# Performance work log

Measured on AMD Instinct MI355X. Metric: run time of the kernel, lower is better.

Reference implementation:

```python
import jax, jax.numpy as jnp
import numpy as np

H = 256    # hidden_size
CVQ = 64   # vq_ph_channel
K = 128    # vq_ph_codebook_dim
NL = 5     # num_layers per ConvBlocks
NB = 2     # layers_in_block
KS = 3     # kernel_size


def _ln_c(x, g, b, eps=1e-5):
    # LayerNorm over channel dim of a [B, C, T] tensor
    m = jnp.mean(x, axis=1, keepdims=True)
    v = jnp.mean((x - m) ** 2, axis=1, keepdims=True)
    return (x - m) * jax.lax.rsqrt(v + eps) * g[None, :, None] + b[None, :, None]


def _causal_conv(x, w, b):
    # x [B,Cin,T], w [Cout,Cin,K]; left (causal) padding of K-1
    y = jax.lax.conv_general_dilated(x, w, (1,), [(w.shape[-1] - 1, 0)],
                                     dimension_numbers=('NCH', 'OIH', 'NCH'))
    return y + b[None, :, None]


def _pw(x, w, b):
    # pointwise (kernel-size-1) conv: w [Cout, Cin]
    return jnp.einsum('oi,bit->bot', w, x) + b[None, :, None]


def _conv_blocks(x, mask, ln_g, ln_b, w1, b1, w2, b2, last_g, last_b, post_w, post_b):
    # LeftPadConvBlocks: NL residual blocks x NB sub-blocks of
    # LN -> causal conv (C->2C, k=3) -> *k^-0.5 -> GELU -> 1x1 conv (2C->C), residual + mask
    scale = KS ** -0.5
    for i in range(NL):
        for j in range(NB):
            h = _ln_c(x, ln_g[i, j], ln_b[i, j])
            h = _causal_conv(h, w1[i, j], b1[i, j]) * scale
            h = jax.nn.gelu(h, approximate=False)
            h = _pw(h, w2[i, j], b2[i, j])
            x = (x + h) * mask
    x = _ln_c(x, last_g, last_b) * mask
    x = _causal_conv(x, post_w, post_b) * mask
    return x


def _group_by_segs(h_bct, mel2ph, L):
    # scatter-mean mel frames into phoneme segments; index 0 = padding (dropped)
    h = jnp.swapaxes(h_bct, 1, 2)  # [B, T, H]
    def one(hb, mb):
        s = jnp.zeros((L + 1, hb.shape[-1]), hb.dtype).at[mb].add(hb)
        c = jnp.zeros((L + 1,), hb.dtype).at[mb].add(1.0)
        return s[1:] / jnp.clip(c[1:], 1.0)[:, None]
    g = jax.vmap(one)(h, mel2ph)   # [B, L, H]
    return jnp.swapaxes(g, 1, 2)   # [B, H, L]


def _vq(z, codebook, beta=0.25):
    # EMA-VQ forward math: nearest-codebook lookup + straight-through + commitment loss
    x = jnp.swapaxes(z, 1, 2)                                # [B, T, C]
    d = (jnp.sum(x ** 2, -1, keepdims=True)
         - 2.0 * jnp.einsum('btc,kc->btk', x, codebook)
         + jnp.sum(codebook ** 2, -1))                       # [B, T, K]
    idx = jnp.argmin(d, axis=-1)                             # [B, T]
    q = codebook[idx]                                        # [B, T, C]
    loss = beta * jnp.mean((x - jax.lax.stop_gradient(q)) ** 2)
    q_st = x + jax.lax.stop_gradient(q - x)
    return jnp.swapaxes(q_st, 1, 2), loss, idx


def setup_inputs() -> dict:
    key = jax.random.key(0)
    ks = list(jax.random.split(key, 64))
    it = iter(ks)
    B, T, L = 16, 2048, 512
    f = lambda shape, s: jax.random.normal(next(it), shape, jnp.float32) * s
    inp = {}
    inp['x'] = jax.random.normal(next(it), (B, 80, T), jnp.float32)
    inp['in_nonpadding'] = jnp.ones((B, 1, T), jnp.float32)
    inp['in_mel2ph'] = jnp.sort(jax.random.randint(next(it), (B, T), 1, L + 1), axis=-1)
    inp['ph_nonpadding'] = jnp.ones((B, 1, L), jnp.float32)
    inp['conv_in_w'] = f((H, 80), 0.05)
    inp['conv_in_b'] = jnp.zeros((H,), jnp.float32)
    for p in ('enc', 'pn'):
        inp[p + '_ln_g'] = jnp.ones((NL, NB, H), jnp.float32)
        inp[p + '_ln_b'] = jnp.zeros((NL, NB, H), jnp.float32)
        inp[p + '_w1'] = f((NL, NB, 2 * H, H, KS), 0.03)
        inp[p + '_b1'] = jnp.zeros((NL, NB, 2 * H), jnp.float32)
        inp[p + '_w2'] = f((NL, NB, H, 2 * H), 0.03)
        inp[p + '_b2'] = jnp.zeros((NL, NB, H), jnp.float32)
        inp[p + '_last_g'] = jnp.ones((H,), jnp.float32)
        inp[p + '_last_b'] = jnp.zeros((H,), jnp.float32)
        inp[p + '_post_w'] = f((H, H, KS), 0.03)
        inp[p + '_post_b'] = jnp.zeros((H,), jnp.float32)
    inp['proj_in_w'] = f((CVQ, H), 0.05)
    inp['proj_in_b'] = jnp.zeros((CVQ,), jnp.float32)
    inp['proj_out_w'] = f((H, CVQ), 0.05)
    inp['proj_out_b'] = jnp.zeros((H,), jnp.float32)
    inp['codebook'] = f((K, CVQ), 0.1)
    return inp


def reference(x, in_nonpadding, in_mel2ph, ph_nonpadding,
              conv_in_w, conv_in_b,
              enc_ln_g, enc_ln_b, enc_w1, enc_b1, enc_w2, enc_b2,
              enc_last_g, enc_last_b, enc_post_w, enc_post_b,
              pn_ln_g, pn_ln_b, pn_w1, pn_b1, pn_w2, pn_b2,
              pn_last_g, pn_last_b, pn_post_w, pn_post_b,
              proj_in_w, proj_in_b, proj_out_w, proj_out_b, codebook):
    L = ph_nonpadding.shape[-1]
    h = _pw(x, conv_in_w, conv_in_b) * in_nonpadding                     # ph_conv_in
    h = _conv_blocks(h, in_nonpadding, enc_ln_g, enc_ln_b, enc_w1, enc_b1,
                     enc_w2, enc_b2, enc_last_g, enc_last_b,
                     enc_post_w, enc_post_b) * in_nonpadding             # ph_encoder
    h = _group_by_segs(h, in_mel2ph, L)                                  # [B, H, L]
    h = _conv_blocks(h, ph_nonpadding, pn_ln_g, pn_ln_b, pn_w1, pn_b1,
                     pn_w2, pn_b2, pn_last_g, pn_last_b,
                     pn_post_w, pn_post_b) * ph_nonpadding               # ph_postnet
    z = _pw(h, proj_in_w, proj_in_b)                                     # ph_latents_proj_in
    q, vq_loss, idx = _vq(z, codebook)                                   # VQ
    out = _pw(q, proj_out_w, proj_out_b)                                 # ph_latents_proj_out
    return out, vq_loss, idx
```

## Files before the change

kernel.cpp:

```cpp
#include <hip/hip_runtime.h>
#include <hip/hip_bf16.h>


typedef unsigned short u16;
typedef unsigned int u32;
typedef __attribute__((ext_vector_type(8))) _Float16 f16x8;
typedef __attribute__((ext_vector_type(16))) float f32x16;

#define OUT_LOSS_OFF 2097152
#define OUT_IDX_OFF  2097153

__device__ __forceinline__ void split_f16(float x, u16& h, u16& l) {
    union { _Float16 f; u16 u; } a, b;
    a.f = (_Float16)x;
    float hf = (float)a.f;
    b.f = (_Float16)(x - hf);
    h = a.u; l = b.u;
}

__global__ __launch_bounds__(256) void k_t_mat(const float* __restrict__ w,
                                               float* __restrict__ wt,
                                               int G, int O, int I) {
    size_t n = (size_t)G * O * I;
    for (size_t i = (size_t)blockIdx.x * 256 + threadIdx.x; i < n;
         i += (size_t)gridDim.x * 256) {
        int ci = (int)(i % I);
        int o  = (int)((i / I) % O);
        int g  = (int)(i / ((size_t)I * O));
        wt[((size_t)g * I + ci) * O + o] = w[i];
    }
}

__global__ __launch_bounds__(256) void k_t_w1mf(const float* __restrict__ w,
                                                u16* __restrict__ BH,
                                                u16* __restrict__ BL, int S) {
    size_t N = (size_t)S * 3 * 16 * 16 * 64 * 8;
    for (size_t i = (size_t)blockIdx.x * 256 + threadIdx.x; i < N;
         i += (size_t)gridDim.x * 256) {
        int j = (int)(i & 7); size_t r = i >> 3;
        int L = (int)(r & 63); r >>= 6;
        int nt = (int)(r & 15); r >>= 4;
        int kb = (int)(r & 15); r >>= 4;
        int k3 = (int)(r % 3); int s = (int)(r / 3);
        int oc = nt * 32 + (L & 31);
        int c = kb * 16 + ((L >> 5) << 3) + j;
        float v = w[(((size_t)s * 512 + oc) * 256 + c) * 3 + k3];
        u16 h, l; split_f16(v, h, l);
        BH[i] = h; BL[i] = l;
    }
}

__global__ __launch_bounds__(256) void k_t_w2mf(const float* __restrict__ w,
                                                u16* __restrict__ BH,
                                                u16* __restrict__ BL, int S) {
    size_t N = (size_t)S * 32 * 8 * 64 * 8;
    for (size_t i = (size_t)blockIdx.x * 256 + threadIdx.x; i < N;
         i += (size_t)gridDim.x * 256) {
        int j = (int)(i & 7);
        int L = (int)((i >> 3) & 63);
        int nt = (int)((i >> 9) & 7);
        int kb = (int)((i >> 12) & 31);
        int s = (int)(i >> 17);
        int oc = nt * 32 + (L & 31);
        int ic = kb * 16 + ((L >> 5) << 3) + j;
        float v = w[((size_t)s * 256 + oc) * 512 + ic];
        u16 h, l; split_f16(v, h, l);
        BH[i] = h; BL[i] = l;
    }
}

// ... 18 lines not shown
                                            const float* __restrict__ wt,
                                            const float* __restrict__ bias,
                                            const float* __restrict__ mask,
                                            float* __restrict__ y,
                                            float* __restrict__ MM,
                                            float* __restrict__ IV, int T) {
    extern __shared__ float X[];
    constexpr int NG = COUT / CHUNK;
    __shared__ float rs[64 * NG], rs2[64 * NG];
    const int b = blockIdx.y, t0 = blockIdx.x * 64;
    for (int i = threadIdx.x; i < CIN * 64; i += 256) {
        int ci = i >> 6, j = i & 63;
        X[i] = x[((size_t)b * CIN + ci) * T + t0 + j];
    }
    __syncthreads();
    const int tl = threadIdx.x & 63;
    const int g = __builtin_amdgcn_readfirstlane((int)(threadIdx.x >> 6));
    float acc[CHUNK];
#pragma unroll
    for (int o = 0; o < CHUNK; o++) acc[o] = 0.f;
    for (int i = 0; i < CIN; i++) {
        float xv = X[i * 64 + tl];
        const float* wr = wt + (size_t)i * COUT + g * CHUNK;
#pragma unroll
        for (int o = 0; o < CHUNK; o++) acc[o] = fmaf(wr[o], xv, acc[o]);
    }
    float mk = mask ? mask[(size_t)b * T + t0 + tl] : 1.0f;
    float s = 0.f, s2 = 0.f;
#pragma unroll
    for (int o = 0; o < CHUNK; o++) {
        int oc = g * CHUNK + o;
        float val = (acc[o] + bias[oc]) * mk;
        y[((size_t)b * COUT + oc) * T + t0 + tl] = val;
        s += val; s2 += val * val;
    }
    if constexpr (STATS) {
        rs[g * 64 + tl] = s; rs2[g * 64 + tl] = s2;
        __syncthreads();
        if (threadIdx.x < 64) {
            float ss = 0.f, ss2 = 0.f;
#pragma unroll
            for (int gg = 0; gg < NG; gg++) {
                ss += rs[gg * 64 + threadIdx.x];
                ss2 += rs2[gg * 64 + threadIdx.x];
            }
            float m = ss * (1.0f / COUT);
            float var = ss2 * (1.0f / COUT) - m * m;
            MM[(size_t)b * T + t0 + threadIdx.x] = m;
            IV[(size_t)b * T + t0 + threadIdx.x] = 1.0f / sqrtf(var + 1e-5f);
        }
    }
}

template <int M>
__global__ __launch_bounds__(512, 4) void k_sub(
    const float* __restrict__ xin, float* __restrict__ xout,
    const float* __restrict__ MMi, const float* __restrict__ IVi,
    const float* __restrict__ lng, const float* __restrict__ lnb,
    const u16* __restrict__ B1H, const u16* __restrict__ B1L,
    const float* __restrict__ b1,
    const u16* __restrict__ B2H, const u16* __restrict__ B2L,
    const float* __restrict__ b2, const float* __restrict__ mask,
    float* __restrict__ MMo, float* __restrict__ IVo, int T) {
    constexpr int MT = M / 32;
    constexpr int SH = (M + 2) * 264 * 2;
    constexpr int CG = 512 / M;
    constexpr int CPT = 256 / CG;
    __shared__ __align__(16) char smem[2 * SH + 4096];
    u16* LH = (u16*)smem;
    u16* LL = (u16*)(smem + SH);
    u16* GH = (u16*)smem;
    u16* GL = (u16*)(smem + SH);
    float* SOUT = (float*)smem;
    float* rs  = (float*)(smem + 2 * SH);
    float* rs2 = (float*)(smem + 2 * SH + 2048);

    const int tid = threadIdx.x;
    const int b = blockIdx.y, t0 = blockIdx.x * M;
    const size_t xoff = (size_t)b * 256 * T;
    const size_t bT = (size_t)b * T;

    {
        int jj = tid & (M - 1);
        int cg = tid / M;
        int t = t0 - 2 + jj;
        bool ok = (t >= 0);
        float m = ok ? MMi[bT + t] : 0.f;
        float v = ok ? IVi[bT + t] : 0.f;
#pragma unroll
        for (int i = 0; i < CPT; i++) {
            int c = cg + i * CG;
            float xv = ok ? xin[xoff + (size_t)c * T + t] : 0.f;
            float ln = ok ? ((xv - m) * v * lng[c] + lnb[c]) : 0.f;
            u16 h, l; split_f16(ln, h, l);
            LH[jj * 264 + c] = h; LL[jj * 264 + c] = l;
        }
        int j2 = M + (tid >> 8);
        int c2 = tid & 255;
        int t2 = t0 + (M - 2) + (tid >> 8);
        float m2 = MMi[bT + t2], v2 = IVi[bT + t2];
        float x2 = xin[xoff + (size_t)c2 * T + t2];
        float ln2 = (x2 - m2) * v2 * lng[c2] + lnb[c2];
        u16 h2, l2; split_f16(ln2, h2, l2);
        LH[j2 * 264 + c2] = h2; LL[j2 * 264 + c2] = l2;
    }
    __syncthreads();

    const int lane = tid & 63;
    const int w = tid >> 6;
    const int arow = lane & 31;
    const int acol = (lane >> 5) << 3;
    const int thalf = (lane >> 5) << 2;
    const float ks = 0.5773502691896258f;
    const int oc_l = w * 32 + (lane & 31);
    const u16* b1h0 = B1H + (size_t)w * 512 + (size_t)lane * 8;
    const u16* b1l0 = B1L + (size_t)w * 512 + (size_t)lane * 8;
    const u16* b1h1 = B1H + (size_t)(8 + w) * 512 + (size_t)lane * 8;
    const u16* b1l1 = B1L + (size_t)(8 + w) * 512 + (size_t)lane * 8;
    const u16* b2h = B2H + (size_t)w * 512 + (size_t)lane * 8;
    const u16* b2l = B2L + (size_t)w * 512 + (size_t)lane * 8;

    f32x16 c0[MT], c1[MT];
#pragma unroll
    for (int m = 0; m < MT; m++)
#pragma unroll
        for (int r = 0; r < 16; r++) { c0[m][r] = 0.f; c1[m][r] = 0.f; }
    __builtin_amdgcn_s_setprio(1);
#pragma unroll 2
    for (int kk = 0; kk < 48; kk++) {
        int k3 = kk >> 4, kb = kk & 15;
        f16x8 bh0 = *(const f16x8*)(b1h0 + (size_t)kk * 8192);
        f16x8 bl0 = *(const f16x8*)(b1l0 + (size_t)kk * 8192);
        f16x8 bh1 = *(const f16x8*)(b1h1 + (size_t)kk * 8192);
        f16x8 bl1 = *(const f16x8*)(b1l1 + (size_t)kk * 8192);
#pragma unroll
        for (int m = 0; m < MT; m++) {
            int ao = (m * 32 + arow + k3) * 264 + kb * 16 + acol;
            f16x8 ah = *(const f16x8*)&LH[ao];
            f16x8 al = *(const f16x8*)&LL[ao];
            c0[m] = __builtin_amdgcn_mfma_f32_32x32x16_f16(ah, bh0, c0[m], 0, 0, 0);
            c1[m] = __builtin_amdgcn_mfma_f32_32x32x16_f16(ah, bh1, c1[m], 0, 0, 0);
            c0[m] = __builtin_amdgcn_mfma_f32_32x32x16_f16(ah, bl0, c0[m], 0, 0, 0);
            c1[m] = __builtin_amdgcn_mfma_f32_32x32x16_f16(ah, bl1, c1[m], 0, 0, 0);
            c0[m] = __builtin_amdgcn_mfma_f32_32x32x16_f16(al, bh0, c0[m], 0, 0, 0);
            c1[m] = __builtin_amdgcn_mfma_f32_32x32x16_f16(al, bh1, c1[m], 0, 0, 0);
        }
    }
    __builtin_amdgcn_s_setprio(0);
    __syncthreads();

    {
        float bb = b1[oc_l];
#pragma unroll
        for (int m = 0; m < MT; m++)
#pragma unroll
            for (int r = 0; r < 16; r++) {
                int trow = m * 32 + thalf + ((r >> 2) << 3) + (r & 3);
                float y = (c0[m][r] + bb) * ks;
                float ge = 0.5f * y * (1.0f + erff(y * 0.7071067811865476f));
                u16 h, l; split_f16(ge, h, l);
                GH[trow * 264 + oc_l] = h; GL[trow * 264 + oc_l] = l;
            }
    }
    __syncthreads();

#pragma unroll
    for (int m = 0; m < MT; m++)
#pragma unroll
        for (int r = 0; r < 16; r++) c0[m][r] = 0.f;
    __builtin_amdgcn_s_setprio(1);
#pragma unroll 2
    for (int i = 0; i < 16; i++) {
        f16x8 bh2 = *(const f16x8*)(b2h + (size_t)i * 4096);
        f16x8 bl2 = *(const f16x8*)(b2l + (size_t)i * 4096);
#pragma unroll
        for (int m = 0; m < MT; m++) {
            int go = (m * 32 + arow) * 264 + i * 16 + acol;
            f16x8 gh = *(const f16x8*)&GH[go];
            f16x8 gl = *(const f16x8*)&GL[go];
            c0[m] = __builtin_amdgcn_mfma_f32_32x32x16_f16(gh, bh2, c0[m], 0, 0, 0);
            c0[m] = __builtin_amdgcn_mfma_f32_32x32x16_f16(gh, bl2, c0[m], 0, 0, 0);
            c0[m] = __builtin_amdgcn_mfma_f32_32x32x16_f16(gl, bh2, c0[m], 0, 0, 0);
        }
    }
    __builtin_amdgcn_s_setprio(0);
    __syncthreads();

    {
        float bb = b1[256 + oc_l];
#pragma unroll
        for (int m = 0; m < MT; m++)
#pragma unroll
            for (int r = 0; r < 16; r++) {
                int trow = m * 32 + thalf + ((r >> 2) << 3) + (r & 3);
                float y = (c1[m][r] + bb) * ks;
                float ge = 0.5f * y * (1.0f + erff(y * 0.7071067811865476f));
                u16 h, l; split_f16(ge, h, l);
                GH[trow * 264 + oc_l] = h; GL[trow * 264 + oc_l] = l;
            }
    }
    __syncthreads();

    __builtin_amdgcn_s_setprio(1);
#pragma unroll 2
    for (int i = 0; i < 16; i++) {
        f16x8 bh2 = *(const f16x8*)(b2h + (size_t)(16 + i) * 4096);
        f16x8 bl2 = *(const f16x8*)(b2l + (size_t)(16 + i) * 4096);
#pragma unroll
        for (int m = 0; m < MT; m++) {
            int go = (m * 32 + arow) * 264 + i * 16 + acol;
            f16x8 gh = *(const f16x8*)&GH[go];
            f16x8 gl = *(const f16x8*)&GL[go];
            c0[m] = __builtin_amdgcn_mfma_f32_32x32x16_f16(gh, bh2, c0[m], 0, 0, 0);
            c0[m] = __builtin_amdgcn_mfma_f32_32x32x16_f16(gh, bl2, c0[m], 0, 0, 0);
            c0[m] = __builtin_amdgcn_mfma_f32_32x32x16_f16(gl, bh2, c0[m], 0, 0, 0);
        }
    }
    __builtin_amdgcn_s_setprio(0);
    __syncthreads();

#pragma unroll
    for (int m = 0; m < MT; m++)
#pragma unroll
        for (int r = 0; r < 16; r++) {
            int trow = m * 32 + thalf + ((r >> 2) << 3) + (r & 3);
            SOUT[trow * 260 + oc_l] = c0[m][r];
        }
    __syncthreads();
    {
        int t = tid & (M - 1), cg = tid / M;
        float mk = mask[bT + t0 + t];
        float s = 0.f, s2 = 0.f;
#pragma unroll
        for (int i = 0; i < CPT; i++) {
            int c = cg * CPT + i;
            size_t adr = xoff + (size_t)c * T + t0 + t;
            float val = (xin[adr] + SOUT[t * 260 + c] + b2[c]) * mk;
            xout[adr] = val;
            s += val; s2 += val * val;
        }
        rs[tid] = s; rs2[tid] = s2;
    }
    __syncthreads();
    if (tid < M) {
        float ss = 0.f, ss2 = 0.f;
#pragma unroll
        for (int k = 0; k < CG; k++) {
            ss += rs[k * M + tid]; ss2 += rs2[k * M + tid];
        }
        float m = ss * (1.0f / 256.0f);
        float var = ss2 * (1.0f / 256.0f) - m * m;
        MMo[bT + t0 + tid] = m;
        IVo[bT + t0 + tid] = 1.0f / sqrtf(var + 1e-5f);
    }
}

__global__ __launch_bounds__(1024, 4) void k_sub16(
    const float* __restrict__ xin, float* __restrict__ xout,
    const float* __restrict__ MMi, const float* __restrict__ IVi,
    const float* __restrict__ lng, const float* __restrict__ lnb,
    const u16* __restrict__ B1H, const u16* __restrict__ B1L,
    const float* __restrict__ b1,
    const u16* __restrict__ B2H, const u16* __restrict__ B2L,
    const float* __restrict__ b2, const float* __restrict__ mask,
    float* __restrict__ MMo, float* __restrict__ IVo, int T) {
    __shared__ __align__(16) char smem[44096];
    u16* LH = (u16*)smem;
    u16* LL = (u16*)(smem + 17952);
    u16* GH = (u16*)smem;
    u16* GL = (u16*)(smem + 17952);
    float* SOUT = (float*)smem;
    float* rs  = (float*)(smem + 35904);
    float* rs2 = (float*)(smem + 40000);

    const int tid = threadIdx.x;
    const int b = blockIdx.y, t0 = blockIdx.x * 32;
    const size_t xoff = (size_t)b * 256 * T;
    const size_t bT = (size_t)b * T;

    {
        int jj = tid & 31;
        int cg = tid >> 5;
        int t = t0 - 2 + jj;
        bool ok = (t >= 0);
        float m = ok ? MMi[bT + t] : 0.f;
        float v = ok ? IVi[bT + t] : 0.f;
#pragma unroll
        for (int i = 0; i < 8; i++) {
            int c = cg + i * 32;
            float xv = ok ? xin[xoff + (size_t)c * T + t] : 0.f;
            float ln = ok ? ((xv - m) * v * lng[c] + lnb[c]) : 0.f;
            u16 h, l; split_f16(ln, h, l);
            LH[jj * 264 + c] = h; LL[jj * 264 + c] = l;
        }
        if (tid < 512) {
            int j2 = 32 + (tid >> 8);
            int c2 = tid & 255;
            int t2 = t0 + 30 + (tid >> 8);
            float ln2 = (xin[xoff + (size_t)c2 * T + t2] - MMi[bT + t2]) *
                        IVi[bT + t2] * lng[c2] + lnb[c2];
            u16 h2, l2; split_f16(ln2, h2, l2);
            LH[j2 * 264 + c2] = h2; LL[j2 * 264 + c2] = l2;
        }
    }
    __syncthreads();

    const int lane = tid & 63;
    const int w = tid >> 6;
    const int arow = lane & 31;
    const int acol = (lane >> 5) << 3;
    const int thalf = (lane >> 5) << 2;
    const float ks = 0.5773502691896258f;
    const int oc_l = w * 32 + (lane & 31);
    const u16* b1h = B1H + (size_t)w * 512 + (size_t)lane * 8;
    const u16* b1l = B1L + (size_t)w * 512 + (size_t)lane * 8;

    f32x16 cc;
#pragma unroll
    for (int r = 0; r < 16; r++) cc[r] = 0.f;
    __builtin_amdgcn_s_setprio(1);
#pragma unroll 4
    for (int kk = 0; kk < 48; kk++) {
        int k3 = kk >> 4, kb = kk & 15;
        int ao = (arow + k3) * 264 + kb * 16 + acol;
        f16x8 ah = *(const f16x8*)&LH[ao];
        f16x8 al = *(const f16x8*)&LL[ao];
        f16x8 bh = *(const f16x8*)(b1h + (size_t)kk * 8192);
        f16x8 bl = *(const f16x8*)(b1l + (size_t)kk * 8192);
        cc = __builtin_amdgcn_mfma_f32_32x32x16_f16(ah, bh, cc, 0, 0, 0);
        cc = __builtin_amdgcn_mfma_f32_32x32x16_f16(ah, bl, cc, 0, 0, 0);
        cc = __builtin_amdgcn_mfma_f32_32x32x16_f16(al, bh, cc, 0, 0, 0);
    }
    __builtin_amdgcn_s_setprio(0);
    __syncthreads();

    u32 preg[16];
    {
        float bb = b1[oc_l];
        if (w < 8) {
#pragma unroll
            for (int r = 0; r < 16; r++) {
                int trow = thalf + ((r >> 2) << 3) + (r & 3);
                float y = (cc[r] + bb) * ks;
                float ge = 0.5f * y * (1.0f + erff(y * 0.7071067811865476f));
                u16 h, l; split_f16(ge, h, l);
                GH[trow * 264 + oc_l] = h; GL[trow * 264 + oc_l] = l;
            }
        } else {
#pragma unroll
            for (int r = 0; r < 16; r++) {
                float y = (cc[r] + bb) * ks;
                float ge = 0.5f * y * (1.0f + erff(y * 0.7071067811865476f));
                u16 h, l; split_f16(ge, h, l);
                preg[r] = ((u32)h << 16) | (u32)l;
            }
        }
    }
    __syncthreads();

    const u16* b2h = B2H + (size_t)(w & 7) * 512 + (size_t)lane * 8;
    const u16* b2l = B2L + (size_t)(w & 7) * 512 + (size_t)lane * 8;
    if (w < 8) {
#pragma unroll
        for (int r = 0; r < 16; r++) cc[r] = 0.f;
        __builtin_amdgcn_s_setprio(1);
#pragma unroll 2
        for (int i = 0; i < 16; i++) {
            int go = arow * 264 + i * 16 + acol;
            f16x8 gh = *(const f16x8*)&GH[go];
            f16x8 gl = *(const f16x8*)&GL[go];
            f16x8 bh2 = *(const f16x8*)(b2h + (size_t)i * 4096);
            f16x8 bl2 = *(const f16x8*)(b2l + (size_t)i * 4096);
            cc = __builtin_amdgcn_mfma_f32_32x32x16_f16(gh, bh2, cc, 0, 0, 0);
            cc = __builtin_amdgcn_mfma_f32_32x32x16_f16(gh, bl2, cc, 0, 0, 0);
            cc = __builtin_amdgcn_mfma_f32_32x32x16_f16(gl, bh2, cc, 0, 0, 0);
        }
        __builtin_amdgcn_s_setprio(0);
    }
    __syncthreads();

    if (w >= 8) {
        int col = oc_l - 256;
#pragma unroll
        for (int r = 0; r < 16; r++) {
            int trow = thalf + ((r >> 2) << 3) + (r & 3);
            GH[trow * 264 + col] = (u16)(preg[r] >> 16);
            GL[trow * 264 + col] = (u16)(preg[r] & 0xffff);
        }
    }
    __syncthreads();

    if (w < 8) {
        __builtin_amdgcn_s_setprio(1);
#pragma unroll 2
        for (int i = 0; i < 16; i++) {
            int go = arow * 264 + i * 16 + acol;
            f16x8 gh = *(const f16x8*)&GH[go];
            f16x8 gl = *(const f16x8*)&GL[go];
            f16x8 bh2 = *(const f16x8*)(b2h + (size_t)(16 + i) * 4096);
            f16x8 bl2 = *(const f16x8*)(b2l + (size_t)(16 + i) * 4096);
            cc = __builtin_amdgcn_mfma_f32_32x32x16_f16(gh, bh2, cc, 0, 0, 0);
            cc = __builtin_amdgcn_mfma_f32_32x32x16_f16(gh, bl2, cc, 0, 0, 0);
            cc = __builtin_amdgcn_mfma_f32_32x32x16_f16(gl, bh2, cc, 0, 0, 0);
        }
        __builtin_amdgcn_s_setprio(0);
    }
    __syncthreads();

    if (w < 8) {
#pragma unroll
        for (int r = 0; r < 16; r++) {
            int trow = thalf + ((r >> 2) << 3) + (r & 3);
            SOUT[trow * 260 + oc_l] = cc[r];
        }
    }
    __syncthreads();
    {
        int t = tid & 31, cg = tid >> 5;
        float mk = mask[bT + t0 + t];
        float s = 0.f, s2 = 0.f;
#pragma unroll
        for (int i = 0; i < 8; i++) {
            int c = cg * 8 + i;
            size_t adr = xoff + (size_t)c * T + t0 + t;
            float val = (xin[adr] + SOUT[t * 260 + c] + b2[c]) * mk;
            xout[adr] = val;
            s += val; s2 += val * val;
        }
        rs[tid] = s; rs2[tid] = s2;
    }
    __syncthreads();
    if (tid < 32) {
        float ss = 0.f, ss2 = 0.f;
#pragma unroll
        for (int k = 0; k < 32; k++) {
            ss += rs[k * 32 + tid]; ss2 += rs2[k * 32 + tid];
        }
        float m = ss * (1.0f / 256.0f);
        float var = ss2 * (1.0f / 256.0f) - m * m;
        MMo[bT + t0 + tid] = m;
        IVo[bT + t0 + tid] = 1.0f / sqrtf(var + 1e-5f);
    }
}

template <int M>
__global__ __launch_bounds__(512, (M == 32 ? 8 : 4)) void k_lnc(
    const float* __restrict__ xin, float* __restrict__ xout,
    const float* __restrict__ MM, const float* __restrict__ IV,
    const float* __restrict__ lg, const float* __restrict__ lb,
    const u16* __restrict__ BH, const u16* __restrict__ BL,
    const float* __restrict__ bias, const float* __restrict__ mask, int T) {
    constexpr int MT = M / 32;
    constexpr int SH = (M + 2) * 264 * 2;
    constexpr int CG = 512 / M;
    constexpr int CPT = 256 / CG;
    __shared__ __align__(16) char smem[2 * SH];
    u16* LH = (u16*)smem;
    u16* LL = (u16*)(smem + SH);
    float* SOUT = (float*)smem;

    const int tid = threadIdx.x;
    const int b = blockIdx.y, t0 = blockIdx.x * M;
    const size_t xoff = (size_t)b * 256 * T;
    const size_t bT = (size_t)b * T;

    {
// ... 242 lines not shown
    const float* proj_out_b = (const float*)d_in[29];
    const float* codebook   = (const float*)d_in[30];
    float* out = (float*)d_out;

    float* ws = (float*)d_ws;
    float* A      = ws;
    float* Bb     = A + 8388608;
    float* CINT   = Bb + 8388608;
    float* PINT   = CINT + 20480;
    float* POUTT  = PINT + 16384;
    float* Z      = POUTT + 16384;
    float* MM0    = Z + 524288;
    float* IV0    = MM0 + 32768;
    float* MM1    = IV0 + 32768;
    float* IV1    = MM1 + 32768;
    int*   CNT    = (int*)(IV1 + 32768);
    int*   IDX    = CNT + 8192;
    float* LOSS   = (float*)(IDX + 8192);
    u16*   BH1E   = (u16*)(LOSS + 64);
    u16*   BL1E   = BH1E + 3932160;
    u16*   BH1P   = BL1E + 3932160;
    u16*   BL1P   = BH1P + 3932160;
    u16*   BH2E   = BL1P + 3932160;
    u16*   BL2E   = BH2E + 1310720;
    u16*   BH2P   = BL2E + 1310720;
    u16*   BL2P   = BH2P + 1310720;
    u16*   PH_E   = BL2P + 1310720;
    u16*   PL_E   = PH_E + 196608;
    u16*   PH_P   = PL_E + 196608;
    u16*   PL_P   = PH_P + 196608;

    k_t_w1mf<<<dim3(4096), dim3(256), 0, stream>>>(e_w1, BH1E, BL1E, 10);
    k_t_w1mf<<<dim3(4096), dim3(256), 0, stream>>>(p_w1, BH1P, BL1P, 10);
    k_t_w2mf<<<dim3(2048), dim3(256), 0, stream>>>(e_w2, BH2E, BL2E, 10);
    k_t_w2mf<<<dim3(2048), dim3(256), 0, stream>>>(p_w2, BH2P, BL2P, 10);
    k_t_wpmf<<<dim3(768),  dim3(256), 0, stream>>>(e_pw, PH_E, PL_E);
    k_t_wpmf<<<dim3(768),  dim3(256), 0, stream>>>(p_pw, PH_P, PL_P);
    k_t_mat  <<<dim3(80),  dim3(256), 0, stream>>>(conv_in_w, CINT, 1, 256, 80);
    k_t_mat  <<<dim3(64),  dim3(256), 0, stream>>>(proj_in_w, PINT, 1, 64, 256);
    k_t_mat  <<<dim3(64),  dim3(256), 0, stream>>>(proj_out_w, POUTT, 1, 256, 64);

    const size_t sm_scat = 256 * 65 * sizeof(float) + 64 * sizeof(int);

    k_pw<80, 256, 64, true><<<dim3(32, 16), dim3(256), 80 * 64 * 4, stream>>>(
        x, CINT, conv_in_b, in_np, A, MM0, IV0, 2048);

    float* cur = A;
    float* nxt = Bb;
    for (int s = 0; s < 10; s++) {
        float* mi = (s & 1) ? MM1 : MM0;
        float* vi = (s & 1) ? IV1 : IV0;
        float* mo = (s & 1) ? MM0 : MM1;
        float* vo = (s & 1) ? IV0 : IV1;
        k_sub<64><<<dim3(32, 16), dim3(512), 0, stream>>>(
            cur, nxt, mi, vi, e_ln_g + s * 256, e_ln_b + s * 256,
            BH1E + (size_t)s * 393216, BL1E + (size_t)s * 393216, e_b1 + s * 512,
            BH2E + (size_t)s * 131072, BL2E + (size_t)s * 131072, e_b2 + s * 256,
            in_np, mo, vo, 2048);
        float* t = cur; cur = nxt; nxt = t;
    }
    k_lnc<64><<<dim3(32, 16), dim3(512), 0, stream>>>(
        cur, nxt, MM0, IV0, e_lg, e_lb, PH_E, PL_E, e_pb, in_np, 2048);

    hipMemsetAsync(A, 0, (size_t)2097152 * 4, stream);
    hipMemsetAsync(LOSS, 0, 4, stream);
    k_counts<<<dim3(16), dim3(256), 0, stream>>>(mel2ph, CNT);
    k_scatter<<<dim3(32, 16), dim3(256), sm_scat, stream>>>(Bb, mel2ph, A);
    k_postprep<<<dim3(16), dim3(512), 0, stream>>>(A, CNT, MM0, IV0);

    cur = A; nxt = Bb;
    for (int s = 0; s < 10; s++) {
        float* mi = (s & 1) ? MM1 : MM0;
        float* vi = (s & 1) ? IV1 : IV0;
        float* mo = (s & 1) ? MM0 : MM1;
        float* vo = (s & 1) ? IV0 : IV1;
        k_sub16<<<dim3(16, 16), dim3(1024), 0, stream>>>(
            cur, nxt, mi, vi, p_ln_g + s * 256, p_ln_b + s * 256,
            BH1P + (size_t)s * 393216, BL1P + (size_t)s * 393216, p_b1 + s * 512,
            BH2P + (size_t)s * 131072, BL2P + (size_t)s * 131072, p_b2 + s * 256,
            ph_np, mo, vo, 512);
        float* t = cur; cur = nxt; nxt = t;
    }
    k_lnc<32><<<dim3(16, 16), dim3(512), 0, stream>>>(
        cur, nxt, MM0, IV0, p_lg, p_lb, PH_P, PL_P, p_pb, ph_np, 512);

    k_pw<256, 64, 16, false><<<dim3(8, 16), dim3(256), 256 * 64 * 4, stream>>>(
        Bb, PINT, proj_in_b, nullptr, Z, nullptr, nullptr, 512);

    k_vq<<<dim3(32), dim3(256), 0, stream>>>(Z, codebook, IDX, out, LOSS);
    k_loss<<<dim3(1), dim3(64), 0, stream>>>(LOSS, out);
    k_projout<<<dim3(8, 16), dim3(256), 0, stream>>>(codebook, IDX, POUTT,
                                                     proj_out_b, out);
}
```

Measured before the change: 2.119 ms.

## Interleave GELU packing with MFMA phases and split second GEMM across all waves

The 64-row sub-block kernel is specialised and reordered so the GELU and f16 hi/lo packing of one accumulator tile runs inside the MFMA loop that computes the next tile. This overlaps transcendental and LDS-store work with matrix-core work and removes separate barrier-delimited GELU passes. The 32-row kernel now stores the whole 512-wide GELU output in LDS and has all 16 waves do half of the K reduction of the 1x1 conv, adding the partials in LDS, instead of leaving half the waves idle. In exchange, the 32-row kernel's LDS footprint grows, which can lower blocks per CU, and it adds an extra accumulate pass through LDS.

```diff
diff --git a/kernel.cpp b/kernel.cpp
--- a/kernel.cpp
+++ b/kernel.cpp
@@ -16,6 +16,15 @@
     float hf = (float)a.f;
     b.f = (_Float16)(x - hf);
     h = a.u; l = b.u;
+}
+
+__device__ __forceinline__ void gelu_pack(float v, float bb, u16* GH, u16* GL,
+                                          int off) {
+    const float ks = 0.5773502691896258f;
+    float y = (v + bb) * ks;
+    float ge = 0.5f * y * (1.0f + erff(y * 0.7071067811865476f));
+    u16 h, l; split_f16(ge, h, l);
+    GH[off] = h; GL[off] = l;
 }
 
 __global__ __launch_bounds__(256) void k_t_mat(const float* __restrict__ w,
@@ -140,8 +149,7 @@
     }
 }
 
-template <int M>
-__global__ __launch_bounds__(512, 4) void k_sub(
+__global__ __launch_bounds__(512, 4) void k_sub64(
     const float* __restrict__ xin, float* __restrict__ xout,
     const float* __restrict__ MMi, const float* __restrict__ IVi,
     const float* __restrict__ lng, const float* __restrict__ lnb,
@@ -150,42 +158,38 @@
     const u16* __restrict__ B2H, const u16* __restrict__ B2L,
     const float* __restrict__ b2, const float* __restrict__ mask,
     float* __restrict__ MMo, float* __restrict__ IVo, int T) {
-    constexpr int MT = M / 32;
-    constexpr int SH = (M + 2) * 264 * 2;
-    constexpr int CG = 512 / M;
-    constexpr int CPT = 256 / CG;
-    __shared__ __align__(16) char smem[2 * SH + 4096];
+    __shared__ __align__(16) char smem[73792];
     u16* LH = (u16*)smem;
-    u16* LL = (u16*)(smem + SH);
+    u16* LL = (u16*)(smem + 34848);
     u16* GH = (u16*)smem;
-    u16* GL = (u16*)(smem + SH);
+    u16* GL = (u16*)(smem + 34848);
     float* SOUT = (float*)smem;
-    float* rs  = (float*)(smem + 2 * SH);
-    float* rs2 = (float*)(smem + 2 * SH + 2048);
+    float* rs  = (float*)(smem + 69696);
+    float* rs2 = (float*)(smem + 71744);
 
     const int tid = threadIdx.x;
-    const int b = blockIdx.y, t0 = blockIdx.x * M;
+    const int b = blockIdx.y, t0 = blockIdx.x * 64;
     const size_t xoff = (size_t)b * 256 * T;
     const size_t bT = (size_t)b * T;
 
     {
-        int jj = tid & (M - 1);
-        int cg = tid / M;
+        int jj = tid & 63;
+        int cg = tid >> 6;
         int t = t0 - 2 + jj;
         bool ok = (t >= 0);
         float m = ok ? MMi[bT + t] : 0.f;
         float v = ok ? IVi[bT + t] : 0.f;
 #pragma unroll
-        for (int i = 0; i < CPT; i++) {
-            int c = cg + i * CG;
+        for (int i = 0; i < 32; i++) {
+            int c = cg + i * 8;
             float xv = ok ? xin[xoff + (size_t)c * T + t] : 0.f;
             float ln = ok ? ((xv - m) * v * lng[c] + lnb[c]) : 0.f;
             u16 h, l; split_f16(ln, h, l);
             LH[jj * 264 + c] = h; LL[jj * 264 + c] = l;
         }
-        int j2 = M + (tid >> 8);
+        int j2 = 64 + (tid >> 8);
         int c2 = tid & 255;
-        int t2 = t0 + (M - 2) + (tid >> 8);
+        int t2 = t0 + 62 + (tid >> 8);
         float m2 = MMi[bT + t2], v2 = IVi[bT + t2];
         float x2 = xin[xoff + (size_t)c2 * T + t2];
         float ln2 = (x2 - m2) * v2 * lng[c2] + lnb[c2];
@@ -199,7 +203,6 @@
     const int arow = lane & 31;
     const int acol = (lane >> 5) << 3;
     const int thalf = (lane >> 5) << 2;
-    const float ks = 0.5773502691896258f;
     const int oc_l = w * 32 + (lane & 31);
     const u16* b1h0 = B1H + (size_t)w * 512 + (size_t)lane * 8;
     const u16* b1l0 = B1L + (size_t)w * 512 + (size_t)lane * 8;
@@ -207,121 +210,157 @@
     const u16* b1l1 = B1L + (size_t)(8 + w) * 512 + (size_t)lane * 8;
     const u16* b2h = B2H + (size_t)w * 512 + (size_t)lane * 8;
     const u16* b2l = B2L + (size_t)w * 512 + (size_t)lane * 8;
-
-    f32x16 c0[MT], c1[MT];
-#pragma unroll
-    for (int m = 0; m < MT; m++)
-#pragma unroll
-        for (int r = 0; r < 16; r++) { c0[m][r] = 0.f; c1[m][r] = 0.f; }
+    const float bb0 = b1[oc_l];
+    const float bb1 = b1[256 + oc_l];
+
+    f32x16 c00, c10;
+#pragma unroll
+    for (int r = 0; r < 16; r++) { c00[r] = 0.f; c10[r] = 0.f; }
     __builtin_amdgcn_s_setprio(1);
 #pragma unroll 2
     for (int kk = 0; kk < 48; kk++) {
         int k3 = kk >> 4, kb = kk & 15;
+        int ao = (arow + k3) * 264 + kb * 16 + acol;
+        f16x8 ah = *(const f16x8*)&LH[ao];
+        f16x8 al = *(const f16x8*)&LL[ao];
         f16x8 bh0 = *(const f16x8*)(b1h0 + (size_t)kk * 8192);
         f16x8 bl0 = *(const f16x8*)(b1l0 + (size_t)kk * 8192);
         f16x8 bh1 = *(const f16x8*)(b1h1 + (size_t)kk * 8192);
         f16x8 bl1 = *(const f16x8*)(b1l1 + (size_t)kk * 8192);
-#pragma unroll
-        for (int m = 0; m < MT; m++) {
-            int ao = (m * 32 + arow + k3) * 264 + kb * 16 + acol;
+        c00 = __builtin_amdgcn_mfma_f32_32x32x16_f16(ah, bh0, c00, 0, 0, 0);
+        c10 = __builtin_amdgcn_mfma_f32_32x32x16_f16(ah, bh1, c10, 0, 0, 0);
+        c00 = __builtin_amdgcn_mfma_f32_32x32x16_f16(ah, bl0, c00, 0, 0, 0);
+        c10 = __builtin_amdgcn_mfma_f32_32x32x16_f16(ah, bl1, c10, 0, 0, 0);
+        c00 = __builtin_amdgcn_mfma_f32_32x32x16_f16(al, bh0, c00, 0, 0, 0);
+        c10 = __builtin_amdgcn_mfma_f32_32x32x16_f16(al, bh1, c10, 0, 0, 0);
+    }
+    __builtin_amdgcn_s_setprio(0);
+    __syncthreads();
+
+    f32x16 c01, c11;
+#pragma unroll
+    for (int r = 0; r < 16; r++) { c01[r] = 0.f; c11[r] = 0.f; }
+    __builtin_amdgcn_s_setprio(1);
+#pragma unroll
+    for (int g = 0; g < 16; g++) {
+#pragma unroll
+        for (int t3 = 0; t3 < 3; t3++) {
+            int kk = g * 3 + t3;
+            int k3 = kk >> 4, kb = kk & 15;
+            int ao = (32 + arow + k3) * 264 + kb * 16 + acol;
             f16x8 ah = *(const f16x8*)&LH[ao];
             f16x8 al = *(const f16x8*)&LL[ao];
-            c0[m] = __builtin_amdgcn_mfma_f32_32x32x16_f16(ah, bh0, c0[m], 0, 0, 0);
-            c1[m] = __builtin_amdgcn_mfma_f32_32x32x16_f16(ah, bh1, c1[m], 0, 0, 0);
-            c0[m] = __builtin_amdgcn_mfma_f32_32x32x16_f16(ah, bl0, c0[m], 0, 0, 0);
-            c1[m] = __builtin_amdgcn_mfma_f32_32x32x16_f16(ah, bl1, c1[m], 0, 0, 0);
-            c0[m] = __builtin_amdgcn_mfma_f32_32x32x16_f16(al, bh0, c0[m], 0, 0, 0);
-            c1[m] = __builtin_amdgcn_mfma_f32_32x32x16_f16(al, bh1, c1[m], 0, 0, 0);
+            f16x8 bh0 = *(const f16x8*)(b1h0 + (size_t)kk * 8192);
+            f16x8 bl0 = *(const f16x8*)(b1l0 + (size_t)kk * 8192);
+            f16x8 bh1 = *(const f16x8*)(b1h1 + (size_t)kk * 8192);
+            f16x8 bl1 = *(const f16x8*)(b1l1 + (size_t)kk * 8192);
+            c01 = __builtin_amdgcn_mfma_f32_32x32x16_f16(ah, bh0, c01, 0, 0, 0);
+            c11 = __builtin_amdgcn_mfma_f32_32x32x16_f16(ah, bh1, c11, 0, 0, 0);
+            c01 = __builtin_amdgcn_mfma_f32_32x32x16_f16(ah, bl0, c01, 0, 0, 0);
+            c11 = __builtin_amdgcn_mfma_f32_32x32x16_f16(ah, bl1, c11, 0, 0, 0);
+            c01 = __builtin_amdgcn_mfma_f32_32x32x16_f16(al, bh0, c01, 0, 0, 0);
+            c11 = __builtin_amdgcn_mfma_f32_32x32x16_f16(al, bh1, c11, 0, 0, 0);
+        }
+        {
+            int trow = thalf + ((g >> 2) << 3) + (g & 3);
+            gelu_pack(c00[g], bb0, GH, GL, trow * 264 + oc_l);
         }
     }
     __builtin_amdgcn_s_setprio(0);
     __syncthreads();
 
-    {
-        float bb = b1[oc_l];
-#pragma unroll
-        for (int m = 0; m < MT; m++)
-#pragma unroll
-            for (int r = 0; r < 16; r++) {
-                int trow = m * 32 + thalf + ((r >> 2) << 3) + (r & 3);
-                float y = (c0[m][r] + bb) * ks;
-                float ge = 0.5f * y * (1.0f + erff(y * 0.7071067811865476f));
-                u16 h, l; split_f16(ge, h, l);
-                GH[trow * 264 + oc_l] = h; GL[trow * 264 + oc_l] = l;
-            }
-    }
-    __syncthreads();
-
-#pragma unroll
-    for (int m = 0; m < MT; m++)
-#pragma unroll
-        for (int r = 0; r < 16; r++) c0[m][r] = 0.f;
+    f32x16 a0;
+#pragma unroll
+    for (int r = 0; r < 16; r++) a0[r] = 0.f;
     __builtin_amdgcn_s_setprio(1);
-#pragma unroll 2
+#pragma unroll
     for (int i = 0; i < 16; i++) {
+        int go = arow * 264 + i * 16 + acol;
+        f16x8 gh = *(const f16x8*)&GH[go];
+        f16x8 gl = *(const f16x8*)&GL[go];
         f16x8 bh2 = *(const f16x8*)(b2h + (size_t)i * 4096);
         f16x8 bl2 = *(const f16x8*)(b2l + (size_t)i * 4096);
-#pragma unroll
-        for (int m = 0; m < MT; m++) {
-            int go = (m * 32 + arow) * 264 + i * 16 + acol;
-            f16x8 gh = *(const f16x8*)&GH[go];
-            f16x8 gl = *(const f16x8*)&GL[go];
-            c0[m] = __builtin_amdgcn_mfma_f32_32x32x16_f16(gh, bh2, c0[m], 0, 0, 0);
-            c0[m] = __builtin_amdgcn_mfma_f32_32x32x16_f16(gh, bl2, c0[m], 0, 0, 0);
-            c0[m] = __builtin_amdgcn_mfma_f32_32x32x16_f16(gl, bh2, c0[m], 0, 0, 0);
+        a0 = __builtin_amdgcn_mfma_f32_32x32x16_f16(gh, bh2, a0, 0, 0, 0);
+        a0 = __builtin_amdgcn_mfma_f32_32x32x16_f16(gh, bl2, a0, 0, 0, 0);
+        a0 = __builtin_amdgcn_mfma_f32_32x32x16_f16(gl, bh2, a0, 0, 0, 0);
+        {
+            int trow = 32 + thalf + ((i >> 2) << 3) + (i & 3);
+            gelu_pack(c01[i], bb0, GH, GL, trow * 264 + oc_l);
         }
     }
     __builtin_amdgcn_s_setprio(0);
     __syncthreads();
 
-    {
-        float bb = b1[256 + oc_l];
-#pragma unroll
-        for (int m = 0; m < MT; m++)
-#pragma unroll
-            for (int r = 0; r < 16; r++) {
-                int trow = m * 32 + thalf + ((r >> 2) << 3) + (r & 3);
-                float y = (c1[m][r] + bb) * ks;
-                float ge = 0.5f * y * (1.0f + erff(y * 0.7071067811865476f));
-                u16 h, l; split_f16(ge, h, l);
-                GH[trow * 264 + oc_l] = h; GL[trow * 264 + oc_l] = l;
-            }
-    }
-    __syncthreads();
-
+    f32x16 a1;
+#pragma unroll
+    for (int r = 0; r < 16; r++) a1[r] = 0.f;
     __builtin_amdgcn_s_setprio(1);
-#pragma unroll 2
+#pragma unroll
     for (int i = 0; i < 16; i++) {
+        int go = (32 + arow) * 264 + i * 16 + acol;
+        f16x8 gh = *(const f16x8*)&GH[go];
+        f16x8 gl = *(const f16x8*)&GL[go];
+        f16x8 bh2 = *(const f16x8*)(b2h + (size_t)i * 4096);
+        f16x8 bl2 = *(const f16x8*)(b2l + (size_t)i * 4096);
+        a1 = __builtin_amdgcn_mfma_f32_32x32x16_f16(gh, bh2, a1, 0, 0, 0);
+        a1 = __builtin_amdgcn_mfma_f32_32x32x16_f16(gh, bl2, a1, 0, 0, 0);
+        a1 = __builtin_amdgcn_mfma_f32_32x32x16_f16(gl, bh2, a1, 0, 0, 0);
+        {
+            int trow = thalf + ((i >> 2) << 3) + (i & 3);
+            gelu_pack(c10[i], bb1, GH, GL, trow * 264 + oc_l);
+        }
+    }
+    __builtin_amdgcn_s_setprio(0);
+    __syncthreads();
+
+    __builtin_amdgcn_s_setprio(1);
+#pragma unroll
+    for (int i = 0; i < 16; i++) {
+        int go = arow * 264 + i * 16 + acol;
+        f16x8 gh = *(const f16x8*)&GH[go];
+        f16x8 gl = *(const f16x8*)&GL[go];
         f16x8 bh2 = *(const f16x8*)(b2h + (size_t)(16 + i) * 4096);
         f16x8 bl2 = *(const f16x8*)(b2l + (size_t)(16 + i) * 4096);
-#pragma unroll
-        for (int m = 0; m < MT; m++) {
-            int go = (m * 32 + arow) * 264 + i * 16 + acol;
-            f16x8 gh = *(const f16x8*)&GH[go];
-            f16x8 gl = *(const f16x8*)&GL[go];
-            c0[m] = __builtin_amdgcn_mfma_f32_32x32x16_f16(gh, bh2, c0[m], 0, 0, 0);
-            c0[m] = __builtin_amdgcn_mfma_f32_32x32x16_f16(gh, bl2, c0[m], 0, 0, 0);
-            c0[m] = __builtin_amdgcn_mfma_f32_32x32x16_f16(gl, bh2, c0[m], 0, 0, 0);
+        a0 = __builtin_amdgcn_mfma_f32_32x32x16_f16(gh, bh2, a0, 0, 0, 0);
+        a0 = __builtin_amdgcn_mfma_f32_32x32x16_f16(gh, bl2, a0, 0, 0, 0);
+        a0 = __builtin_amdgcn_mfma_f32_32x32x16_f16(gl, bh2, a0, 0, 0, 0);
+        {
+            int trow = 32 + thalf + ((i >> 2) << 3) + (i & 3);
+            gelu_pack(c11[i], bb1, GH, GL, trow * 264 + oc_l);
         }
     }
     __builtin_amdgcn_s_setprio(0);
     __syncthreads();
 
-#pragma unroll
-    for (int m = 0; m < MT; m++)
-#pragma unroll
-        for (int r = 0; r < 16; r++) {
-            int trow = m * 32 + thalf + ((r >> 2) << 3) + (r & 3);
-            SOUT[trow * 260 + oc_l] = c0[m][r];
-        }
+    __builtin_amdgcn_s_setprio(1);
+#pragma unroll 4
+    for (int i = 0; i < 16; i++) {
+        int go = (32 + arow) * 264 + i * 16 + acol;
+        f16x8 gh = *(const f16x8*)&GH[go];
+        f16x8 gl = *(const f16x8*)&GL[go];
+        f16x8 bh2 = *(const f16x8*)(b2h + (size_t)(16 + i) * 4096);
+        f16x8 bl2 = *(const f16x8*)(b2l + (size_t)(16 + i) * 4096);
+        a1 = __builtin_amdgcn_mfma_f32_32x32x16_f16(gh, bh2, a1, 0, 0, 0);
+        a1 = __builtin_amdgcn_mfma_f32_32x32x16_f16(gh, bl2, a1, 0, 0, 0);
+        a1 = __builtin_amdgcn_mfma_f32_32x32x16_f16(gl, bh2, a1, 0, 0, 0);
+    }
+    __builtin_amdgcn_s_setprio(0);
+    __syncthreads();
+
+#pragma unroll
+    for (int r = 0; r < 16; r++) {
+        int trow = thalf + ((r >> 2) << 3) + (r & 3);
+        SOUT[trow * 260 + oc_l] = a0[r];
+        SOUT[(32 + trow) * 260 + oc_l] = a1[r];
+    }
     __syncthreads();
     {
-        int t = tid & (M - 1), cg = tid / M;
+        int t = tid & 63, cg = tid >> 6;
         float mk = mask[bT + t0 + t];
         float s = 0.f, s2 = 0.f;
 #pragma unroll
-        for (int i = 0; i < CPT; i++) {
-            int c = cg * CPT + i;
+        for (int i = 0; i < 32; i++) {
+            int c = cg * 32 + i;
             size_t adr = xoff + (size_t)c * T + t0 + t;
             float val = (xin[adr] + SOUT[t * 260 + c] + b2[c]) * mk;
             xout[adr] = val;
@@ -330,11 +369,11 @@
         rs[tid] = s; rs2[tid] = s2;
     }
     __syncthreads();
-    if (tid < M) {
+    if (tid < 64) {
         float ss = 0.f, ss2 = 0.f;
 #pragma unroll
-        for (int k = 0; k < CG; k++) {
-            ss += rs[k * M + tid]; ss2 += rs2[k * M + tid];
+        for (int k = 0; k < 8; k++) {
+            ss += rs[k * 64 + tid]; ss2 += rs2[k * 64 + tid];
         }
         float m = ss * (1.0f / 256.0f);
         float var = ss2 * (1.0f / 256.0f) - m * m;
@@ -352,14 +391,14 @@
     const u16* __restrict__ B2H, const u16* __restrict__ B2L,
     const float* __restrict__ b2, const float* __restrict__ mask,
     float* __restrict__ MMo, float* __restrict__ IVo, int T) {
-    __shared__ __align__(16) char smem[44096];
+    __shared__ __align__(16) char smem[76800];
     u16* LH = (u16*)smem;
     u16* LL = (u16*)(smem + 17952);
     u16* GH = (u16*)smem;
-    u16* GL = (u16*)(smem + 17952);
+    u16* GL = (u16*)(smem + 34304);
     float* SOUT = (float*)smem;
-    float* rs  = (float*)(smem + 35904);
-    float* rs2 = (float*)(smem + 40000);
+    float* rs  = (float*)(smem + 68608);
+    float* rs2 = (float*)(smem + 72704);
 
     const int tid = threadIdx.x;
     const int b = blockIdx.y, t0 = blockIdx.x * 32;
@@ -398,7 +437,6 @@
     const int arow = lane & 31;
     const int acol = (lane >> 5) << 3;
     const int thalf = (lane >> 5) << 2;
-    const float ks = 0.5773502691896258f;
     const int oc_l = w * 32 + (lane & 31);
     const u16* b1h = B1H + (size_t)w * 512 + (size_t)lane * 8;
     const u16* b1l = B1L + (size_t)w * 512 + (size_t)lane * 8;
@@ -422,77 +460,36 @@
     __builtin_amdgcn_s_setprio(0);
     __syncthreads();
 
-    u32 preg[16];
     {
         float bb = b1[oc_l];
-        if (w < 8) {
-#pragma unroll
-            for (int r = 0; r < 16; r++) {
-                int trow = thalf + ((r >> 2) << 3) + (r & 3);
-                float y = (cc[r] + bb) * ks;
-                float ge = 0.5f * y * (1.0f + erff(y * 0.7071067811865476f));
-                u16 h, l; split_f16(ge, h, l);
-                GH[trow * 264 + oc_l] = h; GL[trow * 264 + oc_l] = l;
-            }
-        } else {
-#pragma unroll
-            for (int r = 0; r < 16; r++) {
-                float y = (cc[r] + bb) * ks;
-                float ge = 0.5f * y * (1.0f + erff(y * 0.7071067811865476f));
-                u16 h, l; split_f16(ge, h, l);
-                preg[r] = ((u32)h << 16) | (u32)l;
-            }
-        }
-    }
-    __syncthreads();
-
-    const u16* b2h = B2H + (size_t)(w & 7) * 512 + (size_t)lane * 8;
-    const u16* b2l = B2L + (size_t)(w & 7) * 512 + (size_t)lane * 8;
-    if (w < 8) {
-#pragma unroll
-        for (int r = 0; r < 16; r++) cc[r] = 0.f;
-        __builtin_amdgcn_s_setprio(1);
-#pragma unroll 2
-        for (int i = 0; i < 16; i++) {
-            int go = arow * 264 + i * 16 + acol;
-            f16x8 gh = *(const f16x8*)&GH[go];
-            f16x8 gl = *(const f16x8*)&GL[go];
-            f16x8 bh2 = *(const f16x8*)(b2h + (size_t)i * 4096);
-            f16x8 bl2 = *(const f16x8*)(b2l + (size_t)i * 4096);
-            cc = __builtin_amdgcn_mfma_f32_32x32x16_f16(gh, bh2, cc, 0, 0, 0);
-            cc = __builtin_amdgcn_mfma_f32_32x32x16_f16(gh, bl2, cc, 0, 0, 0);
-            cc = __builtin_amdgcn_mfma_f32_32x32x16_f16(gl, bh2, cc, 0, 0, 0);
-        }
-        __builtin_amdgcn_s_setprio(0);
-    }
-    __syncthreads();
-
-    if (w >= 8) {
-        int col = oc_l - 256;
 #pragma unroll
         for (int r = 0; r < 16; r++) {
             int trow = thalf + ((r >> 2) << 3) + (r & 3);
-            GH[trow * 264 + col] = (u16)(preg[r] >> 16);
-            GL[trow * 264 + col] = (u16)(preg[r] & 0xffff);
-        }
-    }
-    __syncthreads();
-
-    if (w < 8) {
-        __builtin_amdgcn_s_setprio(1);
-#pragma unroll 2
-        for (int i = 0; i < 16; i++) {
-            int go = arow * 264 + i * 16 + acol;
-            f16x8 gh = *(const f16x8*)&GH[go];
-            f16x8 gl = *(const f16x8*)&GL[go];
-            f16x8 bh2 = *(const f16x8*)(b2h + (size_t)(16 + i) * 4096);
-            f16x8 bl2 = *(const f16x8*)(b2l + (size_t)(16 + i) * 4096);
-            cc = __builtin_amdgcn_mfma_f32_32x32x16_f16(gh, bh2, cc, 0, 0, 0);
-            cc = __builtin_amdgcn_mfma_f32_32x32x16_f16(gh, bl2, cc, 0, 0, 0);
-            cc = __builtin_amdgcn_mfma_f32_32x32x16_f16(gl, bh2, cc, 0, 0, 0);
-        }
-        __builtin_amdgcn_s_setprio(0);
-    }
+            gelu_pack(cc[r], bb, GH, GL, trow * 536 + oc_l);
+        }
+    }
+    __syncthreads();
+
+    const int nt2 = w & 7;
+    const int ih = w >> 3;
+    const u16* b2h = B2H + (size_t)nt2 * 512 + (size_t)lane * 8;
+    const u16* b2l = B2L + (size_t)nt2 * 512 + (size_t)lane * 8;
+#pragma unroll
+    for (int r = 0; r < 16; r++) cc[r] = 0.f;
+    __builtin_amdgcn_s_setprio(1);
+#pragma unroll 4
+    for (int i = 0; i < 16; i++) {
+        int ii = ih * 16 + i;
+        int go = arow * 536 + ii * 16 + acol;
+        f16x8 gh = *(const f16x8*)&GH[go];
+        f16x8 gl = *(const f16x8*)&GL[go];
+        f16x8 bh2 = *(const f16x8*)(b2h + (size_t)ii * 4096);
+        f16x8 bl2 = *(const f16x8*)(b2l + (size_t)ii * 4096);
+        cc = __builtin_amdgcn_mfma_f32_32x32x16_f16(gh, bh2, cc, 0, 0, 0);
+        cc = __builtin_amdgcn_mfma_f32_32x32x16_f16(gh, bl2, cc, 0, 0, 0);
+        cc = __builtin_amdgcn_mfma_f32_32x32x16_f16(gl, bh2, cc, 0, 0, 0);
+    }
+    __builtin_amdgcn_s_setprio(0);
     __syncthreads();
 
     if (w < 8) {
@@ -500,6 +497,15 @@
         for (int r = 0; r < 16; r++) {
             int trow = thalf + ((r >> 2) << 3) + (r & 3);
             SOUT[trow * 260 + oc_l] = cc[r];
+        }
+    }
+    __syncthreads();
+    if (w >= 8) {
+        int oc2 = nt2 * 32 + (lane & 31);
+#pragma unroll
+        for (int r = 0; r < 16; r++) {
+            int trow = thalf + ((r >> 2) << 3) + (r & 3);
+            SOUT[trow * 260 + oc2] += cc[r];
         }
     }
     __syncthreads();
@@ -848,7 +854,7 @@
         float* vi = (s & 1) ? IV1 : IV0;
         float* mo = (s & 1) ? MM0 : MM1;
         float* vo = (s & 1) ? IV0 : IV1;
-        k_sub<64><<<dim3(32, 16), dim3(512), 0, stream>>>(
+        k_sub64<<<dim3(32, 16), dim3(512), 0, stream>>>(
             cur, nxt, mi, vi, e_ln_g + s * 256, e_ln_b + s * 256,
             BH1E + (size_t)s * 393216, BL1E + (size_t)s * 393216, e_b1 + s * 512,
             BH2E + (size_t)s * 131072, BL2E + (size_t)s * 131072, e_b2 + s * 256,
```

New measurement: 2.414 ms. +13.9%, slower.

## Split second GEMM K-dimension across all 16 waves in k_sub16 with LDS reduction

Applied to the files above, without the earlier changes.

In k_sub16, the full 512-wide GELU output now goes into a larger shared-memory buffer, so all 16 waves take part in the 1x1 conv GEMM. Before, only 8 waves did both K halves in sequence while the other 8 sat idle. Each wave half now does one K half, and the partial sums are combined through a two-step accumulate into SOUT. LDS use per block rises from about 44KB to 75KB, which may limit how many blocks fit per CU. It also adds one extra barrier and a read-modify-write pass on shared memory. A GELU helper function is factored out as well.

```diff
diff --git a/kernel.cpp b/kernel.cpp
--- a/kernel.cpp
+++ b/kernel.cpp
@@ -16,6 +16,15 @@
     float hf = (float)a.f;
     b.f = (_Float16)(x - hf);
     h = a.u; l = b.u;
+}
+
+__device__ __forceinline__ void gelu_pack(float v, float bb, u16* GH, u16* GL,
+                                          int off) {
+    const float ks = 0.5773502691896258f;
+    float y = (v + bb) * ks;
+    float ge = 0.5f * y * (1.0f + erff(y * 0.7071067811865476f));
+    u16 h, l; split_f16(ge, h, l);
+    GH[off] = h; GL[off] = l;
 }
 
 __global__ __launch_bounds__(256) void k_t_mat(const float* __restrict__ w,
@@ -199,7 +208,6 @@
     const int arow = lane & 31;
     const int acol = (lane >> 5) << 3;
     const int thalf = (lane >> 5) << 2;
-    const float ks = 0.5773502691896258f;
     const int oc_l = w * 32 + (lane & 31);
     const u16* b1h0 = B1H + (size_t)w * 512 + (size_t)lane * 8;
     const u16* b1l0 = B1L + (size_t)w * 512 + (size_t)lane * 8;
@@ -244,10 +252,7 @@
 #pragma unroll
             for (int r = 0; r < 16; r++) {
                 int trow = m * 32 + thalf + ((r >> 2) << 3) + (r & 3);
-                float y = (c0[m][r] + bb) * ks;
-                float ge = 0.5f * y * (1.0f + erff(y * 0.7071067811865476f));
-                u16 h, l; split_f16(ge, h, l);
-                GH[trow * 264 + oc_l] = h; GL[trow * 264 + oc_l] = l;
+                gelu_pack(c0[m][r], bb, GH, GL, trow * 264 + oc_l);
             }
     }
     __syncthreads();
@@ -281,10 +286,7 @@
 #pragma unroll
             for (int r = 0; r < 16; r++) {
                 int trow = m * 32 + thalf + ((r >> 2) << 3) + (r & 3);
-                float y = (c1[m][r] + bb) * ks;
-                float ge = 0.5f * y * (1.0f + erff(y * 0.7071067811865476f));
-                u16 h, l; split_f16(ge, h, l);
-                GH[trow * 264 + oc_l] = h; GL[trow * 264 + oc_l] = l;
+                gelu_pack(c1[m][r], bb, GH, GL, trow * 264 + oc_l);
             }
     }
     __syncthreads();
@@ -352,14 +354,14 @@
     const u16* __restrict__ B2H, const u16* __restrict__ B2L,
     const float* __restrict__ b2, const float* __restrict__ mask,
     float* __restrict__ MMo, float* __restrict__ IVo, int T) {
-    __shared__ __align__(16) char smem[44096];
+    __shared__ __align__(16) char smem[76800];
     u16* LH = (u16*)smem;
     u16* LL = (u16*)(smem + 17952);
     u16* GH = (u16*)smem;
-    u16* GL = (u16*)(smem + 17952);
+    u16* GL = (u16*)(smem + 34304);
     float* SOUT = (float*)smem;
-    float* rs  = (float*)(smem + 35904);
-    float* rs2 = (float*)(smem + 40000);
+    float* rs  = (float*)(smem + 68608);
+    float* rs2 = (float*)(smem + 72704);
 
     const int tid = threadIdx.x;
     const int b = blockIdx.y, t0 = blockIdx.x * 32;
@@ -398,7 +400,6 @@
     const int arow = lane & 31;
     const int acol = (lane >> 5) << 3;
     const int thalf = (lane >> 5) << 2;
-    const float ks = 0.5773502691896258f;
     const int oc_l = w * 32 + (lane & 31);
     const u16* b1h = B1H + (size_t)w * 512 + (size_t)lane * 8;
     const u16* b1l = B1L + (size_t)w * 512 + (size_t)lane * 8;
@@ -422,77 +423,36 @@
     __builtin_amdgcn_s_setprio(0);
     __syncthreads();
 
-    u32 preg[16];
     {
         float bb = b1[oc_l];
-        if (w < 8) {
-#pragma unroll
-            for (int r = 0; r < 16; r++) {
-                int trow = thalf + ((r >> 2) << 3) + (r & 3);
-                float y = (cc[r] + bb) * ks;
-                float ge = 0.5f * y * (1.0f + erff(y * 0.7071067811865476f));
-                u16 h, l; split_f16(ge, h, l);
-                GH[trow * 264 + oc_l] = h; GL[trow * 264 + oc_l] = l;
-            }
-        } else {
-#pragma unroll
-            for (int r = 0; r < 16; r++) {
-                float y = (cc[r] + bb) * ks;
-                float ge = 0.5f * y * (1.0f + erff(y * 0.7071067811865476f));
-                u16 h, l; split_f16(ge, h, l);
-                preg[r] = ((u32)h << 16) | (u32)l;
-            }
-        }
-    }
-    __syncthreads();
-
-    const u16* b2h = B2H + (size_t)(w & 7) * 512 + (size_t)lane * 8;
-    const u16* b2l = B2L + (size_t)(w & 7) * 512 + (size_t)lane * 8;
-    if (w < 8) {
-#pragma unroll
-        for (int r = 0; r < 16; r++) cc[r] = 0.f;
-        __builtin_amdgcn_s_setprio(1);
-#pragma unroll 2
-        for (int i = 0; i < 16; i++) {
-            int go = arow * 264 + i * 16 + acol;
-            f16x8 gh = *(const f16x8*)&GH[go];
-            f16x8 gl = *(const f16x8*)&GL[go];
-            f16x8 bh2 = *(const f16x8*)(b2h + (size_t)i * 4096);
-            f16x8 bl2 = *(const f16x8*)(b2l + (size_t)i * 4096);
-            cc = __builtin_amdgcn_mfma_f32_32x32x16_f16(gh, bh2, cc, 0, 0, 0);
-            cc = __builtin_amdgcn_mfma_f32_32x32x16_f16(gh, bl2, cc, 0, 0, 0);
-            cc = __builtin_amdgcn_mfma_f32_32x32x16_f16(gl, bh2, cc, 0, 0, 0);
-        }
-        __builtin_amdgcn_s_setprio(0);
-    }
-    __syncthreads();
-
-    if (w >= 8) {
-        int col = oc_l - 256;
 #pragma unroll
         for (int r = 0; r < 16; r++) {
             int trow = thalf + ((r >> 2) << 3) + (r & 3);
-            GH[trow * 264 + col] = (u16)(preg[r] >> 16);
-            GL[trow * 264 + col] = (u16)(preg[r] & 0xffff);
-        }
-    }
-    __syncthreads();
-
-    if (w < 8) {
-        __builtin_amdgcn_s_setprio(1);
-#pragma unroll 2
-        for (int i = 0; i < 16; i++) {
-            int go = arow * 264 + i * 16 + acol;
-            f16x8 gh = *(const f16x8*)&GH[go];
-            f16x8 gl = *(const f16x8*)&GL[go];
-            f16x8 bh2 = *(const f16x8*)(b2h + (size_t)(16 + i) * 4096);
-            f16x8 bl2 = *(const f16x8*)(b2l + (size_t)(16 + i) * 4096);
-            cc = __builtin_amdgcn_mfma_f32_32x32x16_f16(gh, bh2, cc, 0, 0, 0);
-            cc = __builtin_amdgcn_mfma_f32_32x32x16_f16(gh, bl2, cc, 0, 0, 0);
-            cc = __builtin_amdgcn_mfma_f32_32x32x16_f16(gl, bh2, cc, 0, 0, 0);
-        }
-        __builtin_amdgcn_s_setprio(0);
-    }
+            gelu_pack(cc[r], bb, GH, GL, trow * 536 + oc_l);
+        }
+    }
+    __syncthreads();
+
+    const int nt2 = w & 7;
+    const int ih = w >> 3;
+    const u16* b2h = B2H + (size_t)nt2 * 512 + (size_t)lane * 8;
+    const u16* b2l = B2L + (size_t)nt2 * 512 + (size_t)lane * 8;
+#pragma unroll
+    for (int r = 0; r < 16; r++) cc[r] = 0.f;
+    __builtin_amdgcn_s_setprio(1);
+#pragma unroll 4
+    for (int i = 0; i < 16; i++) {
+        int ii = ih * 16 + i;
+        int go = arow * 536 + ii * 16 + acol;
+        f16x8 gh = *(const f16x8*)&GH[go];
+        f16x8 gl = *(const f16x8*)&GL[go];
+        f16x8 bh2 = *(const f16x8*)(b2h + (size_t)ii * 4096);
+        f16x8 bl2 = *(const f16x8*)(b2l + (size_t)ii * 4096);
+        cc = __builtin_amdgcn_mfma_f32_32x32x16_f16(gh, bh2, cc, 0, 0, 0);
+        cc = __builtin_amdgcn_mfma_f32_32x32x16_f16(gh, bl2, cc, 0, 0, 0);
+        cc = __builtin_amdgcn_mfma_f32_32x32x16_f16(gl, bh2, cc, 0, 0, 0);
+    }
+    __builtin_amdgcn_s_setprio(0);
     __syncthreads();
 
     if (w < 8) {
@@ -500,6 +460,15 @@
         for (int r = 0; r < 16; r++) {
             int trow = thalf + ((r >> 2) << 3) + (r & 3);
             SOUT[trow * 260 + oc_l] = cc[r];
+        }
+    }
+    __syncthreads();
+    if (w >= 8) {
+        int oc2 = nt2 * 32 + (lane & 31);
+#pragma unroll
+        for (int r = 0; r < 16; r++) {
+            int trow = thalf + ((r >> 2) << 3) + (r & 3);
+            SOUT[trow * 260 + oc2] += cc[r];
         }
     }
     __syncthreads();
```

Measured after the change: 2.062 ms. -2.7%, faster.
